# Performance work log

Hardware: AMD Instinct MI355X
Metric: run time of the kernel (lower is better)

The kernel has to match this reference:

```python
import jax, jax.numpy as jnp
import numpy as np

N_NODES = 50000
N_EDGES = 800000
NUM_FEATS = 128
HIDDEN = 512
OUT = 2


def setup_inputs() -> dict:
    key = jax.random.key(0)
    k1, k2, k3, k4 = jax.random.split(key, 4)
    X = jax.random.normal(k1, (N_NODES, NUM_FEATS), dtype=jnp.float32)
    edge_index = jax.random.randint(k2, (2, N_EDGES), 0, N_NODES, dtype=jnp.int64)
    W1 = jax.random.normal(k3, (NUM_FEATS, HIDDEN), dtype=jnp.float32) / np.sqrt(NUM_FEATS)
    b1 = jnp.zeros((HIDDEN,), dtype=jnp.float32)
    W2 = jax.random.normal(k4, (HIDDEN, OUT), dtype=jnp.float32) / np.sqrt(HIDDEN)
    b2 = jnp.zeros((OUT,), dtype=jnp.float32)
    return {"X": X, "edge_index": edge_index, "W1": W1, "b1": b1, "W2": W2, "b2": b2}


def _gcn_conv(x, W, b, src, dst, dinv, n):
    # PyG GCNConv: x' = D^{-1/2} (A + I) D^{-1/2} (x W) + b
    xw = x @ W  # [N, C]
    edge_norm = dinv[src] * dinv[dst]  # [E]
    msg = xw[src] * edge_norm[:, None]  # [E, C] gathered messages
    agg = jax.ops.segment_sum(msg, dst, num_segments=n)
    agg = agg + xw * (dinv * dinv)[:, None]  # self-loop contribution
    return agg + b


def reference(X, edge_index, W1, b1, W2, b2):
    n = X.shape[0]
    src, dst = edge_index[0], edge_index[1]
    # degree with self-loops (gcn_norm): deg[i] = in_degree(i) + 1
    deg = jax.ops.segment_sum(jnp.ones_like(dst, dtype=X.dtype), dst, num_segments=n) + 1.0
    dinv = jax.lax.rsqrt(deg)
    h = jax.nn.relu(_gcn_conv(X, W1, b1, src, dst, dinv, n))
    logits = _gcn_conv(h, W2, b2, src, dst, dinv, n)
    # nn.Softmax() on a 2D tensor defaults to dim=1
    return jax.nn.softmax(logits, axis=1)
```

## Files before the change

kernel.cpp:

```cpp
#include <hip/hip_runtime.h>

#define N_FEATS 128
#define HIDDEN 512
#define NPAD 50176
#define NBKT 196
#define SLAB 4608
#define PA_EPB 4096
#define PA_BLOCKS 196
#define XH_BLOCKS 6250

typedef __attribute__((ext_vector_type(4))) float floatx4;
typedef __attribute__((ext_vector_type(8))) short shortx8;
typedef __attribute__((ext_vector_type(8))) unsigned short ushortx8;

__device__ __forceinline__ unsigned short f2bf(float f) {
    union { float f; unsigned u; } a; a.f = f;
    unsigned r = a.u + 0x7fff + ((a.u >> 16) & 1);
    return (unsigned short)(r >> 16);
}
#define BF(x) ({ union { unsigned u; float f; } _c; _c.u = (unsigned)(x) << 16; _c.f; })

__global__ __launch_bounds__(256) void k_initA(const float* __restrict__ W1,
        unsigned short* __restrict__ w1t, const float* __restrict__ X,
        unsigned short* __restrict__ Xh, const int* __restrict__ src,
        const int* __restrict__ dst, int* __restrict__ bcur,
        unsigned* __restrict__ staging, int E, int N) {
    int b = blockIdx.x, tid = threadIdx.x;
    if (b < PA_BLOCKS) {
        __shared__ int hist[NBKT];
        __shared__ int base[NBKT];
        for (int i = tid; i < NBKT; i += 256) hist[i] = 0;
        __syncthreads();
        #pragma unroll
        for (int i = 0; i < 4; ++i) {
            int e = b * PA_EPB + (i * 256 + tid) * 4;
            if (e + 3 < E) {
                int4 d4 = *reinterpret_cast<const int4*>(dst + e);
                atomicAdd(&hist[d4.x >> 8], 1);
                atomicAdd(&hist[d4.y >> 8], 1);
                atomicAdd(&hist[d4.z >> 8], 1);
                atomicAdd(&hist[d4.w >> 8], 1);
            } else {
                for (int k = 0; k < 4; ++k)
                    if (e + k < E) atomicAdd(&hist[dst[e + k] >> 8], 1);
            }
        }
        __syncthreads();
        for (int i = tid; i < NBKT; i += 256) {
            int c = hist[i];
            base[i] = c ? atomicAdd(&bcur[i], c) : 0;
            hist[i] = 0;
        }
        __syncthreads();
        #pragma unroll
        for (int i = 0; i < 4; ++i) {
            int e = b * PA_EPB + (i * 256 + tid) * 4;
            if (e + 3 < E) {
                int4 d4 = *reinterpret_cast<const int4*>(dst + e);
                int4 s4 = *reinterpret_cast<const int4*>(src + e);
                #define PUT(dd, ss) { int bk = (dd) >> 8; int r = atomicAdd(&hist[bk], 1); \
                    int pos = base[bk] + r; if (pos < SLAB) \
                    staging[(size_t)bk * SLAB + pos] = ((unsigned)(ss) << 8) | (unsigned)((dd) & 255); }
                PUT(d4.x, s4.x) PUT(d4.y, s4.y) PUT(d4.z, s4.z) PUT(d4.w, s4.w)
            } else {
                for (int k = 0; k < 4; ++k)
                    if (e + k < E) { int dd = dst[e + k], ss = src[e + k]; PUT(dd, ss) }
                #undef PUT
            }
        }
    } else if (b < PA_BLOCKS + 16) {
        __shared__ unsigned short t[64][65];
        int bb = b - PA_BLOCKS;
        int ki = bb >> 3, ni = bb & 7;
        #pragma unroll
        for (int i = 0; i < 16; ++i) {
            int idx = tid + i * 256;
            int r = idx >> 6, c = idx & 63;
            t[r][c] = f2bf(W1[(ki * 64 + r) * 512 + ni * 64 + c]);
        }
        __syncthreads();
        #pragma unroll
        for (int i = 0; i < 16; ++i) {
            int idx = tid + i * 256;
            int rn = idx >> 6, ck = idx & 63;
            w1t[(ni * 64 + rn) * 128 + ki * 64 + ck] = t[ck][rn];
        }
    } else {
        int idx = (b - PA_BLOCKS - 16) * 256 + tid;
        if (idx < N * 32) {
            float4 v = reinterpret_cast<const float4*>(X)[idx];
            ushort4 o;
            o.x = f2bf(v.x); o.y = f2bf(v.y); o.z = f2bf(v.z); o.w = f2bf(v.w);
            reinterpret_cast<ushort4*>(Xh)[idx] = o;
        }
    }
}

__global__ __launch_bounds__(256) void k_bucketB(const int* __restrict__ bcur,
        const unsigned* __restrict__ staging, int* __restrict__ csr_g,
        int* __restrict__ offs_g, int* __restrict__ cursor, float* __restrict__ dinvs) {
    __shared__ int hist[256];
    __shared__ int offs_l[256];
    __shared__ int sc[256];
    int b = blockIdx.x, tid = threadIdx.x;
    hist[tid] = 0;
    __syncthreads();
    int cnt = bcur[b];
    if (cnt > SLAB) cnt = SLAB;
    const unsigned* st = staging + (size_t)b * SLAB;
    for (int j = tid; j < cnt; j += 256) atomicAdd(&hist[st[j] & 255u], 1);
    __syncthreads();
    int c = hist[tid];
    sc[tid] = c;
    __syncthreads();
    #pragma unroll
    for (int off = 1; off < 256; off <<= 1) {
        int t = (tid >= off) ? sc[tid - off] : 0;
        __syncthreads();
        sc[tid] += t;
        __syncthreads();
    }
    int excl = sc[tid] - c;
    offs_l[tid] = excl;
    int node = (b << 8) + tid;
    cursor[node] = c;
    dinvs[node] = rsqrtf((float)c + 1.0f);
    offs_g[node] = b * SLAB + excl;
    hist[tid] = 0;
    __syncthreads();
    for (int j = tid; j < cnt; j += 256) {
        unsigned v = st[j];
        int dl = (int)(v & 255u);
        int s = (int)(v >> 8);
        int p = atomicAdd(&hist[dl], 1);
        csr_g[b * SLAB + offs_l[dl] + p] = s;
    }
}

__global__ __launch_bounds__(512, 4) void k_gather_gemm(
        const int* __restrict__ cursor, const float* __restrict__ dinvs,
        const int* __restrict__ offs_g, const int* __restrict__ csr_g,
        const unsigned short* __restrict__ Xh, const unsigned short* __restrict__ w1t,
        const float* __restrict__ b1, const float* __restrict__ W2,
        float2* __restrict__ lps, int N) {
    __shared__ unsigned short As[128][136];
    __shared__ unsigned short Bs[128][136];
    __shared__ float b1s[HIDDEN];
    __shared__ float W2s[HIDDEN * 2];

    const int tid = threadIdx.x;
    const int m0 = blockIdx.x * 128;
    for (int i = tid; i < HIDDEN; i += 512) b1s[i] = b1[i];
    for (int i = tid; i < HIDDEN * 2; i += 512) W2s[i] = W2[i];

    union U8 { ushortx8 v; unsigned short s[8]; };

    #pragma unroll
    for (int h = 0; h < 2; ++h) {
        int r = h * 64 + (tid >> 3);
        int lane = tid & 7;
        int gm = m0 + r;
        if (gm < N) {
            float dv = dinvs[gm];
            int beg = offs_g[gm];
            int cnt = cursor[gm];
            const ushortx8* Xp = reinterpret_cast<const ushortx8*>(Xh) + ((size_t)gm << 4);
            U8 sv0, sv1;
            sv0.v = Xp[lane];
            sv1.v = Xp[8 + lane];
            float a0[8], a1[8];
            #pragma unroll
            for (int k = 0; k < 8; ++k) { a0[k] = dv * BF(sv0.s[k]); a1[k] = dv * BF(sv1.s[k]); }
            const int* cp = csr_g + beg;
            int j = 0;
            for (; j + 4 <= cnt; j += 4) {
                int e0 = cp[j], e1 = cp[j + 1], e2 = cp[j + 2], e3 = cp[j + 3];
                float w0 = dinvs[e0], w1 = dinvs[e1], w2 = dinvs[e2], w3 = dinvs[e3];
                const ushortx8* x0 = reinterpret_cast<const ushortx8*>(Xh) + ((size_t)e0 << 4);
                const ushortx8* x1 = reinterpret_cast<const ushortx8*>(Xh) + ((size_t)e1 << 4);
                const ushortx8* x2 = reinterpret_cast<const ushortx8*>(Xh) + ((size_t)e2 << 4);
                const ushortx8* x3 = reinterpret_cast<const ushortx8*>(Xh) + ((size_t)e3 << 4);
                U8 p00, p01, p10, p11, p20, p21, p30, p31;
                p00.v = x0[lane]; p01.v = x0[8 + lane];
                p10.v = x1[lane]; p11.v = x1[8 + lane];
                p20.v = x2[lane]; p21.v = x2[8 + lane];
                p30.v = x3[lane]; p31.v = x3[8 + lane];
                #pragma unroll
                for (int k = 0; k < 8; ++k) {
                    a0[k] += w0 * BF(p00.s[k]) + w1 * BF(p10.s[k]) + w2 * BF(p20.s[k]) + w3 * BF(p30.s[k]);
                    a1[k] += w0 * BF(p01.s[k]) + w1 * BF(p11.s[k]) + w2 * BF(p21.s[k]) + w3 * BF(p31.s[k]);
                }
            }
            for (; j < cnt; ++j) {
                int s = cp[j];
                float w = dinvs[s];
                const ushortx8* xp = reinterpret_cast<const ushortx8*>(Xh) + ((size_t)s << 4);
                U8 q0, q1;
                q0.v = xp[lane]; q1.v = xp[8 + lane];
                #pragma unroll
                for (int k = 0; k < 8; ++k) { a0[k] += w * BF(q0.s[k]); a1[k] += w * BF(q1.s[k]); }
            }
            union { shortx8 v; unsigned short s[8]; } o0, o1;
            #pragma unroll
            for (int k = 0; k < 8; ++k) { o0.s[k] = f2bf(a0[k] * dv); o1.s[k] = f2bf(a1[k] * dv); }
            *reinterpret_cast<shortx8*>(&As[r][lane * 8]) = o0.v;
            *reinterpret_cast<shortx8*>(&As[r][64 + lane * 8]) = o1.v;
        } else {
            shortx8 z = {0, 0, 0, 0, 0, 0, 0, 0};
            *reinterpret_cast<shortx8*>(&As[r][lane * 8]) = z;
            *reinterpret_cast<shortx8*>(&As[r][64 + lane * 8]) = z;
        }
    }
    __syncthreads();

    const int wave = tid >> 6;
    const int lane64 = tid & 63;
    const int quad = lane64 >> 4;
    const int l16 = lane64 & 15;

    float accL0[4] = {0.f, 0.f, 0.f, 0.f};
    float accL1[4] = {0.f, 0.f, 0.f, 0.f};

    for (int n0 = 0; n0 < HIDDEN; n0 += 128) {
        #pragma unroll
        for (int it = 0; it < 4; ++it) {
            int flat = (tid + it * 512) * 8;
            int r = flat >> 7, c = flat & 127;
            *reinterpret_cast<shortx8*>(&Bs[r][c]) =
                *reinterpret_cast<const shortx8*>(w1t + (size_t)(n0 + r) * 128 + c);
        }
        __syncthreads();

        floatx4 acc[8];
        #pragma unroll
        for (int nt = 0; nt < 8; ++nt) acc[nt] = (floatx4){0.f, 0.f, 0.f, 0.f};

        #pragma unroll
        for (int ks = 0; ks < 4; ++ks) {
            shortx8 af = *reinterpret_cast<const shortx8*>(&As[wave * 16 + l16][ks * 32 + quad * 8]);
            #pragma unroll
            for (int nt = 0; nt < 8; ++nt) {
                shortx8 bf = *reinterpret_cast<const shortx8*>(&Bs[nt * 16 + l16][ks * 32 + quad * 8]);
                acc[nt] = __builtin_amdgcn_mfma_f32_16x16x32_bf16(af, bf, acc[nt], 0, 0, 0);
            }
        }

        #pragma unroll
        for (int nt = 0; nt < 8; ++nt) {
            int col = n0 + nt * 16 + l16;
            float bb = b1s[col];
            float w20 = W2s[col * 2 + 0];
            float w21 = W2s[col * 2 + 1];
            #pragma unroll
            for (int r = 0; r < 4; ++r) {
                float hh = acc[nt][r] + bb;
                hh = hh > 0.f ? hh : 0.f;
                accL0[r] += hh * w20;
                accL1[r] += hh * w21;
            }
        }
        __syncthreads();
    }

    #pragma unroll
    for (int off = 1; off < 16; off <<= 1) {
        #pragma unroll
        for (int r = 0; r < 4; ++r) {
            accL0[r] += __shfl_xor(accL0[r], off);
            accL1[r] += __shfl_xor(accL1[r], off);
        }
    }
    if (l16 == 0) {
        #pragma unroll
        for (int r = 0; r < 4; ++r) {
            int gm = m0 + wave * 16 + quad * 4 + r;
            if (gm < N) {
                float dv = dinvs[gm];
                lps[gm] = make_float2(dv * accL0[r], dv * accL1[r]);
            }
        }
    }
}

__global__ __launch_bounds__(256) void k_final(const int* __restrict__ cursor,
        const float* __restrict__ dinvs, const int* __restrict__ offs_g,
        const int* __restrict__ csr_g, const float2* __restrict__ lps,
        const float* __restrict__ b2, float* __restrict__ out, int N) {
    int t = blockIdx.x * 256 + threadIdx.x;
    int node = t >> 3;
    int lane = t & 7;
    if (node >= N) return;
    int cnt = cursor[node];
    int beg = offs_g[node];
    float a0 = 0.f, a1 = 0.f;
    for (int j = lane; j < cnt; j += 8) {
        float2 v = lps[csr_g[beg + j]];
        a0 += v.x;
        a1 += v.y;
    }
    #pragma unroll
    for (int off = 1; off < 8; off <<= 1) {
        a0 += __shfl_xor(a0, off);
        a1 += __shfl_xor(a1, off);
    }
    if (lane == 0) {
        float dv = dinvs[node];
        float2 self = lps[node];
        float l0 = dv * (a0 + self.x) + b2[0];
        float l1 = dv * (a1 + self.y) + b2[1];
        float m = fmaxf(l0, l1);
        float e0 = __expf(l0 - m), e1 = __expf(l1 - m);
        float inv = 1.0f / (e0 + e1);
        out[(size_t)node * 2 + 0] = e0 * inv;
        out[(size_t)node * 2 + 1] = e1 * inv;
    }
}

extern "C" void kernel_launch(void* const* d_in, const int* in_sizes, int n_in,
                              void* d_out, int out_size, void* d_ws, size_t ws_size,
                              hipStream_t stream) {
    const float* X  = (const float*)d_in[0];
    const int* ei   = (const int*)d_in[1];
    const float* W1 = (const float*)d_in[2];
    const float* b1 = (const float*)d_in[3];
    const float* W2 = (const float*)d_in[4];
    const float* b2 = (const float*)d_in[5];
    float* out = (float*)d_out;

    const int N = in_sizes[0] / N_FEATS;
    const int E = in_sizes[1] / 2;
    const int* src = ei;
    const int* dst = ei + E;

    int* cursor  = (int*)d_ws;
    int* bcur    = cursor + NPAD;
    int* offs_g  = bcur + 256;
    float* dinvs = (float*)(offs_g + NPAD);
    float2* lps  = (float2*)(dinvs + NPAD);
    unsigned short* w1t = (unsigned short*)(lps + NPAD);
    unsigned short* Xh  = w1t + 512 * 128;
    unsigned* staging = (unsigned*)(Xh + (size_t)NPAD * 128);
    int* csr_g   = (int*)(staging + (size_t)NBKT * SLAB);

    hipMemsetAsync(bcur, 0, 256 * sizeof(int), stream);
    k_initA      <<<PA_BLOCKS + 16 + XH_BLOCKS, 256, 0, stream>>>(
                     W1, w1t, X, Xh, src, dst, bcur, staging, E, N);
    k_bucketB    <<<NBKT, 256, 0, stream>>>(bcur, staging, csr_g, offs_g, cursor, dinvs);
    k_gather_gemm<<<NPAD / 128, 512, 0, stream>>>(cursor, dinvs, offs_g, csr_g,
                     Xh, w1t, b1, W2, lps, N);
    k_final      <<<((size_t)N * 8 + 255) / 256, 256, 0, stream>>>(
                     cursor, dinvs, offs_g, csr_g, lps, b2, out, N);
}
```

Measured before the change: 151.4 us.

## Drop W1 LDS staging, read B fragments from global, widen gather lanes

```diff
diff --git a/kernel.cpp b/kernel.cpp
--- a/kernel.cpp
+++ b/kernel.cpp
@@ -137,14 +137,13 @@
     }
 }
 
-__global__ __launch_bounds__(512, 4) void k_gather_gemm(
+__global__ __launch_bounds__(512, 6) void k_gather_gemm(
         const int* __restrict__ cursor, const float* __restrict__ dinvs,
         const int* __restrict__ offs_g, const int* __restrict__ csr_g,
         const unsigned short* __restrict__ Xh, const unsigned short* __restrict__ w1t,
         const float* __restrict__ b1, const float* __restrict__ W2,
         float2* __restrict__ lps, int N) {
     __shared__ unsigned short As[128][136];
-    __shared__ unsigned short Bs[128][136];
     __shared__ float b1s[HIDDEN];
     __shared__ float W2s[HIDDEN * 2];
 
@@ -155,60 +154,52 @@
 
     union U8 { ushortx8 v; unsigned short s[8]; };
 
-    #pragma unroll
-    for (int h = 0; h < 2; ++h) {
-        int r = h * 64 + (tid >> 3);
-        int lane = tid & 7;
+    const int lane16 = tid & 15;
+    const int nsub = tid >> 4;
+    const ushortx8* Xv = reinterpret_cast<const ushortx8*>(Xh);
+    #pragma unroll
+    for (int h = 0; h < 4; ++h) {
+        int r = h * 32 + nsub;
         int gm = m0 + r;
         if (gm < N) {
             float dv = dinvs[gm];
             int beg = offs_g[gm];
             int cnt = cursor[gm];
-            const ushortx8* Xp = reinterpret_cast<const ushortx8*>(Xh) + ((size_t)gm << 4);
-            U8 sv0, sv1;
-            sv0.v = Xp[lane];
-            sv1.v = Xp[8 + lane];
-            float a0[8], a1[8];
+            U8 sv; sv.v = Xv[((size_t)gm << 4) + lane16];
+            float a[8];
             #pragma unroll
-            for (int k = 0; k < 8; ++k) { a0[k] = dv * BF(sv0.s[k]); a1[k] = dv * BF(sv1.s[k]); }
+            for (int k = 0; k < 8; ++k) a[k] = dv * BF(sv.s[k]);
             const int* cp = csr_g + beg;
             int j = 0;
+            int4 nxt;
+            if (cnt >= 4) nxt = *reinterpret_cast<const int4*>(cp);
             for (; j + 4 <= cnt; j += 4) {
-                int e0 = cp[j], e1 = cp[j + 1], e2 = cp[j + 2], e3 = cp[j + 3];
-                float w0 = dinvs[e0], w1 = dinvs[e1], w2 = dinvs[e2], w3 = dinvs[e3];
-                const ushortx8* x0 = reinterpret_cast<const ushortx8*>(Xh) + ((size_t)e0 << 4);
-                const ushortx8* x1 = reinterpret_cast<const ushortx8*>(Xh) + ((size_t)e1 << 4);
-                const ushortx8* x2 = reinterpret_cast<const ushortx8*>(Xh) + ((size_t)e2 << 4);
-                const ushortx8* x3 = reinterpret_cast<const ushortx8*>(Xh) + ((size_t)e3 << 4);
-                U8 p00, p01, p10, p11, p20, p21, p30, p31;
-                p00.v = x0[lane]; p01.v = x0[8 + lane];
-                p10.v = x1[lane]; p11.v = x1[8 + lane];
-                p20.v = x2[lane]; p21.v = x2[8 + lane];
-                p30.v = x3[lane]; p31.v = x3[8 + lane];
+                int4 s4 = nxt;
+                if (j + 8 <= cnt) nxt = *reinterpret_cast<const int4*>(cp + j + 4);
+                float w0 = dinvs[s4.x], w1 = dinvs[s4.y], w2 = dinvs[s4.z], w3 = dinvs[s4.w];
+                U8 u0, u1, u2, u3;
+                u0.v = Xv[((size_t)s4.x << 4) + lane16];
+                u1.v = Xv[((size_t)s4.y << 4) + lane16];
+                u2.v = Xv[((size_t)s4.z << 4) + lane16];
+                u3.v = Xv[((size_t)s4.w << 4) + lane16];
                 #pragma unroll
-                for (int k = 0; k < 8; ++k) {
-                    a0[k] += w0 * BF(p00.s[k]) + w1 * BF(p10.s[k]) + w2 * BF(p20.s[k]) + w3 * BF(p30.s[k]);
-                    a1[k] += w0 * BF(p01.s[k]) + w1 * BF(p11.s[k]) + w2 * BF(p21.s[k]) + w3 * BF(p31.s[k]);
-                }
+                for (int k = 0; k < 8; ++k)
+                    a[k] += w0 * BF(u0.s[k]) + w1 * BF(u1.s[k]) + w2 * BF(u2.s[k]) + w3 * BF(u3.s[k]);
             }
             for (; j < cnt; ++j) {
                 int s = cp[j];
                 float w = dinvs[s];
-                const ushortx8* xp = reinterpret_cast<const ushortx8*>(Xh) + ((size_t)s << 4);
-                U8 q0, q1;
-                q0.v = xp[lane]; q1.v = xp[8 + lane];
+                U8 u; u.v = Xv[((size_t)s << 4) + lane16];
                 #pragma unroll
-                for (int k = 0; k < 8; ++k) { a0[k] += w * BF(q0.s[k]); a1[k] += w * BF(q1.s[k]); }
-            }
-            union { shortx8 v; unsigned short s[8]; } o0, o1;
+                for (int k = 0; k < 8; ++k) a[k] += w * BF(u.s[k]);
+            }
+            union { shortx8 v; unsigned short s[8]; } o;
             #pragma unroll
-            for (int k = 0; k < 8; ++k) { o0.s[k] = f2bf(a0[k] * dv); o1.s[k] = f2bf(a1[k] * dv); }
-            *reinterpret_cast<shortx8*>(&As[r][lane * 8]) = o0.v;
-            *reinterpret_cast<shortx8*>(&As[r][64 + lane * 8]) = o1.v;
+            for (int k = 0; k < 8; ++k) o.s[k] = f2bf(a[k] * dv);
+            *reinterpret_cast<shortx8*>(&As[r][lane16 * 8]) = o.v;
         } else {
             shortx8 z = {0, 0, 0, 0, 0, 0, 0, 0};
-            *reinterpret_cast<shortx8*>(&As[r][lane * 8]) = z;
-            *reinterpret_cast<shortx8*>(&As[r][64 + lane * 8]) = z;
+            *reinterpret_cast<shortx8*>(&As[r][lane16 * 8]) = z;
         }
     }
     __syncthreads();
@@ -217,20 +208,13 @@
     const int lane64 = tid & 63;
     const int quad = lane64 >> 4;
     const int l16 = lane64 & 15;
+    const unsigned short* wb = w1t + (size_t)l16 * 128 + quad * 8;
 
     float accL0[4] = {0.f, 0.f, 0.f, 0.f};
     float accL1[4] = {0.f, 0.f, 0.f, 0.f};
 
+    #pragma unroll
     for (int n0 = 0; n0 < HIDDEN; n0 += 128) {
-        #pragma unroll
-        for (int it = 0; it < 4; ++it) {
-            int flat = (tid + it * 512) * 8;
-            int r = flat >> 7, c = flat & 127;
-            *reinterpret_cast<shortx8*>(&Bs[r][c]) =
-                *reinterpret_cast<const shortx8*>(w1t + (size_t)(n0 + r) * 128 + c);
-        }
-        __syncthreads();
-
         floatx4 acc[8];
         #pragma unroll
         for (int nt = 0; nt < 8; ++nt) acc[nt] = (floatx4){0.f, 0.f, 0.f, 0.f};
@@ -240,7 +224,7 @@
             shortx8 af = *reinterpret_cast<const shortx8*>(&As[wave * 16 + l16][ks * 32 + quad * 8]);
             #pragma unroll
             for (int nt = 0; nt < 8; ++nt) {
-                shortx8 bf = *reinterpret_cast<const shortx8*>(&Bs[nt * 16 + l16][ks * 32 + quad * 8]);
+                shortx8 bf = *reinterpret_cast<const shortx8*>(wb + (size_t)(n0 + nt * 16) * 128 + ks * 32);
                 acc[nt] = __builtin_amdgcn_mfma_f32_16x16x32_bf16(af, bf, acc[nt], 0, 0, 0);
             }
         }
@@ -259,7 +243,6 @@
                 accL1[r] += hh * w21;
             }
         }
-        __syncthreads();
     }
 
     #pragma unroll
```

After: 227.1 us. +50.0%, slower.
